# Kernel optimization log

Hardware: AMD Instinct MI355X
Metric: run time of the kernel (lower is better)

Reference implementation:

```python
import jax, jax.numpy as jnp
import numpy as np
from jax.scipy.linalg import cholesky, solve_triangular

SIGMA2 = 0.001   # likelihood.variance (fixed in source)
JITTER = 1e-5


def hankel(v, L):
    # Direct windowed gather; math-identical to the one-hot matmul in the source.
    Nv, Dv = v.shape
    idx = jnp.arange(Nv - L + 1)[:, None] + jnp.arange(L)[None, :]  # [Nv-L+1, L]
    return v[idx].reshape(Nv - L + 1, L * Dv)


def _sqdist(A, B):
    # ||a-b||^2, clipped for numerical safety
    d = jnp.sum(A * A, 1)[:, None] + jnp.sum(B * B, 1)[None, :] - 2.0 * A @ B.T
    return jnp.maximum(d, 0.0)


def _psi_stats(Z, Xmu, Xvar, l2, variance):
    # RBF (ARD) expected-kernel statistics (GPflow conventions).
    N = Xmu.shape[0]
    # psi0: E[k(x,x)] = variance per point, summed over N
    psi0 = jnp.asarray(N, Xmu.dtype) * variance
    # psi1[n,m] = var * prod_q (1+s/l2)^-1/2 * exp(-0.5 (mu-z)^2/(l2+s))
    denom = l2 + Xvar                                        # [N,D]
    logdet1 = -0.5 * jnp.sum(jnp.log1p(Xvar / l2), axis=1)   # [N]
    quad1 = -0.5 * jnp.sum((Xmu[:, None, :] - Z[None, :, :]) ** 2 / denom[:, None, :], axis=2)  # [N,M]
    psi1 = variance * jnp.exp(logdet1[:, None] + quad1)      # [N,M]
    # psi2[n,m,k] = var^2 * prod_q (1+2s/l2)^-1/2
    #   * exp(-(zm-zk)^2/(4 l2) - (mu - (zm+zk)/2)^2 / (2s + l2))
    a = 1.0 / (2.0 * Xvar + l2)                              # [N,D]
    cn = variance ** 2 * jnp.exp(-0.5 * jnp.sum(jnp.log1p(2.0 * Xvar / l2), axis=1))  # [N]
    Zs = Z / (2.0 * jnp.sqrt(l2))
    dZ2 = _sqdist(Zs, Zs)                                    # [M,M], (zm-zk)^2/(4 l2)
    # expand (mu - zbar)^2 * a  without a [N,M,M,D] tensor
    T1 = jnp.sum(a * Xmu * Xmu, axis=1)                      # [N]
    T2 = (a * Xmu) @ Z.T                                     # [N,M]
    T3 = a @ (Z * Z).T                                       # [N,M]
    T4 = jnp.einsum('nq,mq,kq->nmk', a, Z, Z)                # [N,M,M]
    quad2 = (T1[:, None, None] - T2[:, :, None] - T2[:, None, :]
             + 0.25 * (T3[:, :, None] + T3[:, None, :]) + 0.5 * T4)  # [N,M,M]
    psi2 = jnp.sum(cn[:, None, None] * jnp.exp(-dZ2[None, :, :] - quad2), axis=0)  # [M,M]
    return psi0, psi1, psi2


def build_likelihood(X_mean, X_var, Z, lengthscales, variance, Lt):
    N_tot, Q = X_mean.shape
    M = Z.shape[0]
    N = N_tot - Lt
    sigma2 = jnp.asarray(SIGMA2, X_mean.dtype)
    sigma = jnp.sqrt(sigma2)
    l2 = lengthscales ** 2

    X_m = hankel(X_mean[:N_tot - 1], Lt)   # [N, Lt*Q]
    X_v = hankel(X_var[:N_tot - 1], Lt)
    X_mo, X_vo = X_mean[Lt:], X_var[Lt:]   # [N, Q]
    X_mb, X_vb = X_mean[:Lt], X_var[:Lt]   # [Lt, Q]

    Kuu = variance * jnp.exp(-0.5 * _sqdist(Z / lengthscales, Z / lengthscales)) \
          + JITTER * jnp.eye(M, dtype=X_mean.dtype)
    psi0, psi1, psi2 = _psi_stats(Z, X_m, X_v, l2, variance)

    L = cholesky(Kuu, lower=True)
    A = solve_triangular(L, psi1.T, lower=True) / sigma            # [M,N]
    tmp = solve_triangular(L, psi2, lower=True)
    AAT = solve_triangular(L, tmp.T, lower=True) / sigma2          # [M,M]
    B = AAT + jnp.eye(M, dtype=X_mean.dtype)
    LB = cholesky(B, lower=True)
    log_det_B = 2.0 * jnp.sum(jnp.log(jnp.diag(LB)))
    c = solve_triangular(LB, A @ X_mo, lower=True) / sigma         # [M,Q]

    NQ = jnp.asarray(N * Q, X_mean.dtype)
    two_pi = jnp.asarray(2.0 * np.pi, X_mean.dtype)
    ent = 0.5 * jnp.sum(jnp.log(X_vo)) + 0.5 * NQ * jnp.log(two_pi)
    ent2 = -jnp.asarray(Lt * Q, X_mean.dtype) * jnp.log(two_pi) \
           - 0.5 * jnp.sum(X_mb ** 2 + X_vb)

    bound = -0.5 * NQ * jnp.log(two_pi * sigma2)
    bound += -0.5 / sigma2 * (jnp.sum(X_vo) + jnp.sum(X_mo ** 2))
    bound += -0.5 * Q * (psi0 / sigma2 - jnp.trace(AAT))
    bound += -0.5 * Q * log_det_B
    bound += 0.5 * jnp.sum(c ** 2)
    bound += ent + ent2
    return bound


def setup_inputs() -> dict:
    key = jax.random.key(0)
    k1, k2, k3 = jax.random.split(key, 3)
    N, Q, Lt, M = 4096, 4, 8, 128
    D = Lt * Q
    X_mean = jax.random.normal(k1, (N + Lt, Q), dtype=jnp.float32)
    X_var = jax.random.uniform(k2, (N + Lt, Q), dtype=jnp.float32, minval=0.1, maxval=1.0)
    Z = jax.random.normal(k3, (M, D), dtype=jnp.float32)
    lengthscales = 2.0 * jnp.ones((D,), dtype=jnp.float32)
    variance = jnp.asarray(1.0, dtype=jnp.float32)
    return {"X_mean": X_mean, "X_var": X_var, "Z": Z,
            "lengthscales": lengthscales, "variance": variance, "Lt": Lt}


def reference(X_mean, X_var, Z, lengthscales, variance, Lt):
    return build_likelihood(X_mean, X_var, Z, lengthscales, variance, Lt)
```

## Files before the change

### kernel.cpp

```cpp
#include <hip/hip_runtime.h>

#define NN   4096
#define NQ   (NN*4)
#define QQ   4
#define LTT  8
#define DD   32
#define MM   128
#define SIG2 0.001f
#define JIT  1e-5f
#define LOG2E 1.4426950408889634f

typedef _Float16 half8 __attribute__((ext_vector_type(8)));
typedef float    f32x4 __attribute__((ext_vector_type(4)));

__device__ __forceinline__ float fexp2(float x) { return exp2f(x); }

__device__ __forceinline__ float rlane(float v, int l) {
    return __uint_as_float(__builtin_amdgcn_readlane(__float_as_uint(v), l));
}

__global__ __launch_bounds__(256) void k1_kernel(
    const float* __restrict__ Xm, const float* __restrict__ Xv,
    const float* __restrict__ Zg, const float* __restrict__ ls,
    const float* __restrict__ varp,
    _Float16* __restrict__ bh, float* __restrict__ r_g, float* __restrict__ Yg,
    _Float16* __restrict__ Zh, float* __restrict__ Kuu, float* __restrict__ scalars)
{
    int b = blockIdx.x, tid = threadIdx.x;
    if (b < 256) {
        __shared__ float Zl[MM*33];
        __shared__ float pkl[16][DD][4];
        __shared__ float L1l[16], bbl[16];
        __shared__ float lsq[DD];
        __shared__ float yredl[MM*QQ];
        __shared__ float redl[48];
        for (int e = tid; e < MM*DD; e += 256)
            Zl[(e>>5)*33 + (e&31)] = Zg[e];
        if (tid < DD) { float l = ls[tid]; lsq[tid] = 1.0f/(l*l); }
        __syncthreads();
        int n0 = b*16;
        float var  = varp[0];
        float logv = logf(var);
        int nl = tid >> 4;
        int n  = n0 + nl;
        float slog2 = 0.f, slog1 = 0.f, T1 = 0.f, c0 = 0.f;
        #pragma unroll
        for (int t2 = 0; t2 < 2; ++t2) {
            int q = (tid & 15)*2 + t2;
            float xm  = Xm[n*QQ + q];
            float xv  = Xv[n*QQ + q];
            float il2 = lsq[q];
            float l2  = 1.0f / il2;
            float a    = 1.0f / (2.0f*xv + l2);
            float dinv = 1.0f / (l2 + xv);
            pkl[nl][q][0] = LOG2E * a * xm;
            pkl[nl][q][1] = LOG2E * (-0.25f * a);
            pkl[nl][q][2] = dinv;
            pkl[nl][q][3] = -2.0f * dinv * xm;
            bh[n*DD + q] = (_Float16)(0.5f * LOG2E * (il2 - a));
            slog2 += log1pf(2.0f*xv*il2);
            slog1 += log1pf(xv*il2);
            T1    += a*xm*xm;
            c0    += dinv*xm*xm;
        }
        float s1 = 0.f, s2 = 0.f, s3 = 0.f;
        if ((tid & 15) < 4) {
            int c = tid & 3;
            float mo = Xm[(n+LTT)*QQ + c];
            float vo = Xv[(n+LTT)*QQ + c];
            s1 = vo + mo*mo;
            s2 = logf(vo);
            if (n < LTT) {
                float mb = Xm[n*QQ + c], vb = Xv[n*QQ + c];
                s3 = mb*mb + vb;
            }
        }
        #pragma unroll
        for (int off = 1; off < 16; off <<= 1) {
            slog2 += __shfl_xor(slog2, off, 64);
            slog1 += __shfl_xor(slog1, off, 64);
            T1    += __shfl_xor(T1, off, 64);
            c0    += __shfl_xor(c0, off, 64);
            s1    += __shfl_xor(s1, off, 64);
            s2    += __shfl_xor(s2, off, 64);
            s3    += __shfl_xor(s3, off, 64);
        }
        if ((tid & 15) == 0) {
            L1l[nl] = 0.5f * LOG2E * (2.0f*logv - 0.5f*slog2 - T1);
            bbl[nl] = logv - 0.5f*slog1 - 0.5f*c0;
            redl[nl] = s1; redl[16+nl] = s2; redl[32+nl] = s3;
        }
        __syncthreads();
        if (tid == 0) {
            float a1=0.f, a2=0.f, a3=0.f;
            for (int i2 = 0; i2 < 16; ++i2) { a1+=redl[i2]; a2+=redl[16+i2]; a3+=redl[32+i2]; }
            atomicAdd(&scalars[4], a1);
            atomicAdd(&scalars[5], a2);
            atomicAdd(&scalars[6], a3);
        }
        int m = tid & 127, half = tid >> 7;
        float zr[DD];
        #pragma unroll
        for (int q = 0; q < DD; ++q) zr[q] = Zl[m*33 + q];
        float sm = 0.f;
        #pragma unroll
        for (int q = 0; q < DD; ++q) sm = fmaf(zr[q]*zr[q], lsq[q], sm);
        sm *= 0.25f * LOG2E;
        float y0=0.f, y1=0.f, y2=0.f, y3=0.f;
        int nb = half*8;
        for (int i = 0; i < 8; ++i) {
            int nli = nb + i;
            float L1n = L1l[nli], bbn = bbl[nli];
            float racc = 0.f, q1 = 0.f;
            #pragma unroll
            for (int q = 0; q < DD; ++q) {
                float4 v = *(const float4*)&pkl[nli][q][0];
                float z = zr[q];
                racc = fmaf(v.x, z, racc);
                racc = fmaf(v.y, z*z, racc);
                float t = fmaf(v.z, z, v.w);
                q1 = fmaf(t, z, q1);
            }
            int gn = n0 + nli;
            r_g[gn*MM + m] = L1n + racc - sm;
            float p1 = __expf(fmaf(-0.5f, q1, bbn));
            float4 xo = *(const float4*)(Xm + (LTT+gn)*QQ);
            y0 = fmaf(p1, xo.x, y0); y1 = fmaf(p1, xo.y, y1);
            y2 = fmaf(p1, xo.z, y2); y3 = fmaf(p1, xo.w, y3);
        }
        if (half == 0) {
            yredl[m*4+0]=y0; yredl[m*4+1]=y1; yredl[m*4+2]=y2; yredl[m*4+3]=y3;
        }
        __syncthreads();
        if (half == 1) {
            yredl[m*4+0]+=y0; yredl[m*4+1]+=y1; yredl[m*4+2]+=y2; yredl[m*4+3]+=y3;
        }
        __syncthreads();
        for (int e = tid; e < 512; e += 256) atomicAdd(&Yg[e], yredl[e]);
    } else if (b < 320) {
        int idx = (b-256)*256 + tid;
        int i = idx >> 7, j = idx & 127;
        float var = varp[0];
        float s = 0.f;
        for (int q = 0; q < DD; ++q) {
            float l = ls[q];
            float d = (Zg[i*DD+q] - Zg[j*DD+q]) / l;
            s += d*d;
        }
        float v = var * __expf(-0.5f*s);
        if (i == j) v += JIT;
        Kuu[idx] = v;
    } else {
        for (int e = tid; e < MM*DD; e += 256) Zh[e] = (_Float16)Zg[e];
    }
}

__device__ __forceinline__ void dev_chol(float* mat, int tid)
{
    int wv = tid >> 6, ln = tid & 63;
    for (int p = 0; p < 8; ++p) {
        int base = p*16;
        if (wv == 0) {
            int r0 = base + ln, r1 = r0 + 64;
            bool h0 = r0 < 128, h1 = r1 < 128;
            float a0[16], a1[16];
            #pragma unroll
            for (int c = 0; c < 16; ++c) {
                a0[c] = h0 ? mat[r0*132 + base + c] : 0.f;
                a1[c] = h1 ? mat[r1*132 + base + c] : 0.f;
            }
            #pragma unroll
            for (int kk = 0; kk < 16; ++kk) {
                float d   = rlane(a0[kk], kk);
                float rdk = rsqrtf(d);
                float sq  = d * rdk;
                a0[kk] = (ln == kk) ? sq : a0[kk] * rdk;
                a1[kk] *= rdk;
                #pragma unroll
                for (int j = kk+1; j < 16; ++j) {
                    float ljv = rlane(a0[kk], j);
                    a0[j] = fmaf(-a0[kk], ljv, a0[j]);
                    a1[j] = fmaf(-a1[kk], ljv, a1[j]);
                }
            }
            #pragma unroll
            for (int c = 0; c < 16; ++c) {
                if (h0) mat[r0*132 + base + c] = a0[c];
                if (h1) mat[r1*132 + base + c] = a1[c];
            }
        }
        __syncthreads();
        int S = 112 - base;
        if (S > 0) {
            int T = S >> 2, nb = base + 16;
            int nT = (T*(T+1)) >> 1;
            for (int t = tid; t < nT; t += 512) {
                int ti = (int)(0.5f*(sqrtf(8.f*(float)t + 1.f) - 1.f));
                if ((ti+1)*(ti+2)/2 <= t) ++ti;
                else if (ti*(ti+1)/2 > t) --ti;
                int tj = t - ((ti*(ti+1))>>1);
                int i0 = nb + ti*4, j0 = nb + tj*4;
                float ac[4][4];
                #pragma unroll
                for (int r = 0; r < 4; ++r)
                    #pragma unroll
                    for (int s = 0; s < 4; ++s) ac[r][s] = mat[(i0+r)*132 + j0 + s];
                #pragma unroll
                for (int c4 = 0; c4 < 4; ++c4) {
                    float4 av[4], bv[4];
                    #pragma unroll
                    for (int r = 0; r < 4; ++r) {
                        av[r] = *(const float4*)&mat[(i0+r)*132 + base + c4*4];
                        bv[r] = *(const float4*)&mat[(j0+r)*132 + base + c4*4];
                    }
                    #pragma unroll
                    for (int r = 0; r < 4; ++r)
                        #pragma unroll
                        for (int s = 0; s < 4; ++s)
                            ac[r][s] -= av[r].x*bv[s].x + av[r].y*bv[s].y
                                      + av[r].z*bv[s].z + av[r].w*bv[s].w;
                }
                #pragma unroll
                for (int r = 0; r < 4; ++r)
                    #pragma unroll
                    for (int s = 0; s < 4; ++s) mat[(i0+r)*132 + j0 + s] = ac[r][s];
            }
        }
        __syncthreads();
    }
}

__device__ __forceinline__ void dev_dinv(const float* mat, float* dinvb, int tid)
{
    int wv = tid >> 6, ln = tid & 63;
    if (ln < 16) {
        int c = ln, bd = wv;
        int base = bd*16;
        float x[16];
        #pragma unroll
        for (int i = 0; i < 16; ++i) {
            float dii = mat[(base+i)*132 + base + i];
            float s = 0.f;
            #pragma unroll
            for (int j = 0; j < i; ++j) s += mat[(base+i)*132 + base + j] * x[j];
            float v;
            if (i < c) v = 0.f;
            else if (i == c) v = 1.0f / dii;
            else v = -s / dii;
            x[i] = v;
        }
        #pragma unroll
        for (int i = 0; i < 16; ++i) dinvb[bd*256 + i*16 + c] = x[i];
    }
    __syncthreads();
}

__global__ __launch_bounds__(512) void psi2chol_kernel(
    const _Float16* __restrict__ Zh, const float* __restrict__ r_g,
    const _Float16* __restrict__ bh, float* __restrict__ psi2,
    const float* __restrict__ Kuu, float* __restrict__ Lg,
    float* __restrict__ scalars)
{
    __shared__ float shm[19968];
    int tid = threadIdx.x;
    if (blockIdx.x == 0) {
        float* mat   = shm;
        float* dinvb = shm + 16896;
        float* red   = shm + 18944;
        float* tmpM  = shm + 19456;
        for (int e = tid; e < 16384; e += 512) mat[(e>>7)*132 + (e&127)] = Kuu[e];
        __syncthreads();
        dev_chol(mat, tid);
        red[tid] = (tid < 128) ? logf(mat[tid*132 + tid]) : 0.f;
        __syncthreads();
        for (int s = 256; s; s >>= 1) { if (tid < s) red[tid] += red[tid+s]; __syncthreads(); }
        if (tid == 0) scalars[0] = red[0];
        dev_dinv(mat, dinvb, tid);
        #pragma unroll
        for (int bi = 1; bi < 8; ++bi) {
            const int total = bi*256;
            const int np = (total + 511)/512;
            float wbuf[4];
            #pragma unroll
            for (int ps = 0; ps < np; ++ps) {
                int e = ps*512 + tid;
                float Mv = 0.f;
                int bj = e >> 8, r = (e >> 4) & 15, c = e & 15;
                if (e < total) {
                    #pragma unroll
                    for (int kk = 0; kk < 16; ++kk)
                        Mv = fmaf(mat[(bi*16+r)*132 + bj*16+kk], dinvb[bj*256 + kk*16 + c], Mv);
                    for (int k = bj+1; k < bi; ++k)
                        #pragma unroll
                        for (int kk = 0; kk < 16; ++kk)
                            Mv = fmaf(mat[(bi*16+r)*132 + k*16+kk], mat[(k*16+kk)*132 + bj*16+c], Mv);
                }
                __syncthreads();
                if (e < total) tmpM[tid] = Mv;
                __syncthreads();
                float w = 0.f;
                if (e < total) {
                    int lbj = tid >> 8;
                    #pragma unroll
                    for (int kk = 0; kk < 16; ++kk)
                        w = fmaf(dinvb[bi*256 + r*16 + kk], tmpM[lbj*256 + kk*16 + c], w);
                }
                wbuf[ps] = w;
            }
            __syncthreads();
            #pragma unroll
            for (int ps = 0; ps < np; ++ps) {
                int e = ps*512 + tid;
                if (e < total) {
                    int bj = e >> 8, r = (e >> 4) & 15, c = e & 15;
                    mat[(bi*16+r)*132 + bj*16 + c] = -wbuf[ps];
                }
            }
            __syncthreads();
        }
        for (int e = tid; e < 2048; e += 512) {
            int bd = e >> 8, r = (e >> 4) & 15, c = e & 15;
            mat[(bd*16+r)*132 + bd*16 + c] = dinvb[e];
        }
        __syncthreads();
        for (int e = tid; e < 16384; e += 512) Lg[e] = mat[(e>>7)*132 + (e&127)];
    } else {
        float (*pacc)[64][4] = (float(*)[64][4])shm;
        int w = tid >> 6, l = tid & 63, lm = l & 15, lg = l >> 4;
        int b = blockIdx.x - 1;
        int t = b % 36, nq = b / 36;
        int kt = (int)(0.5f*(sqrtf(8.f*(float)t + 1.f) - 1.f));
        if ((kt+1)*(kt+2)/2 <= t) ++kt;
        else if (kt*(kt+1)/2 > t) --kt;
        int mt = t - ((kt*(kt+1))>>1);

        half8 Bf = ((const half8*)Zh)[(kt*16 + lm)*4 + lg];
        half8 Zm = ((const half8*)Zh)[(mt*16 + lm)*4 + lg];
        f32x4 z4; z4[0]=0.f; z4[1]=0.f; z4[2]=0.f; z4[3]=0.f;
        f32x4 acc0 = z4, acc1 = z4;
        int n0g = nq*128 + w*16;
        const float* rbase = r_g + (size_t)n0g*MM;
        const half8* bbase = (const half8*)bh + (size_t)n0g*4;
        for (int i = 0; i < 16; i += 2) {
            half8 bf0 = bbase[i*4 + lg];
            half8 bf1 = bbase[i*4 + 4 + lg];
            const float* rn0 = rbase + i*MM;
            f32x4 rm0 = *(const f32x4*)(rn0 + mt*16 + lg*4);
            f32x4 rm1 = *(const f32x4*)(rn0 + MM + mt*16 + lg*4);
            float rk0 = rn0[kt*16 + lm];
            float rk1 = rn0[MM + kt*16 + lm];
            half8 A0 = Zm * bf0;
            half8 A1 = Zm * bf1;
            f32x4 p0 = __builtin_amdgcn_mfma_f32_16x16x32_f16(A0, Bf, z4, 0, 0, 0);
            f32x4 p1 = __builtin_amdgcn_mfma_f32_16x16x32_f16(A1, Bf, z4, 0, 0, 0);
            acc0[0] += fexp2(p0[0] + rm0[0] + rk0);
            acc0[1] += fexp2(p0[1] + rm0[1] + rk0);
            acc0[2] += fexp2(p0[2] + rm0[2] + rk0);
            acc0[3] += fexp2(p0[3] + rm0[3] + rk0);
            acc1[0] += fexp2(p1[0] + rm1[0] + rk1);
            acc1[1] += fexp2(p1[1] + rm1[1] + rk1);
            acc1[2] += fexp2(p1[2] + rm1[2] + rk1);
            acc1[3] += fexp2(p1[3] + rm1[3] + rk1);
        }
        #pragma unroll
        for (int j = 0; j < 4; ++j) pacc[w][l][j] = acc0[j] + acc1[j];
        __syncthreads();
        if (tid < 256) {
            int ll = tid >> 2, j = tid & 3;
            float s = 0.f;
            #pragma unroll
            for (int ww = 0; ww < 8; ++ww) s += pacc[ww][ll][j];
            int row = mt*16 + (ll >> 4)*4 + j;
            int col = kt*16 + (ll & 15);
            atomicAdd(&psi2[row*MM + col], s);
            if (mt != kt) atomicAdd(&psi2[col*MM + row], s);
        }
    }
}

__global__ __launch_bounds__(512) void cholG_kernel(
    const float* __restrict__ Kuu, const float* __restrict__ psi2,
    const float* __restrict__ Yg, const float* __restrict__ Lg,
    const float* __restrict__ varp,
    float* __restrict__ scalars, int* __restrict__ cnt, float* __restrict__ out)
{
    __shared__ float shm[20480];
    int tid = threadIdx.x;
    if (blockIdx.x == 0) {
        float* mat   = shm;
        float* dinvb = shm + 16896;
        float* rhs   = shm + 18944;
        float* red   = shm + 19456;
        for (int e = tid; e < 16384; e += 512)
            mat[(e>>7)*132 + (e&127)] = Kuu[e] + (1.0f/SIG2)*psi2[e];
        __syncthreads();
        dev_chol(mat, tid);
        red[tid] = (tid < 128) ? logf(mat[tid*132 + tid]) : 0.f;
        __syncthreads();
        for (int s = 256; s; s >>= 1) { if (tid < s) red[tid] += red[tid+s]; __syncthreads(); }
        if (tid == 0) scalars[1] = red[0];
        dev_dinv(mat, dinvb, tid);
        rhs[tid] = Yg[tid];
        __syncthreads();
        if (tid < 64) {
            int r = tid >> 2, cc = tid & 3;
            for (int bi = 0; bi < 8; ++bi) {
                float a0 = rhs[(bi*16+r)*4 + cc], a1 = 0.f, a2 = 0.f, a3 = 0.f;
                for (int bk = 0; bk < bi; ++bk) {
                    const float* mrow = &mat[(bi*16+r)*132 + bk*16];
                    const float* rb   = &rhs[bk*64 + cc];
                    #pragma unroll
                    for (int kk = 0; kk < 16; kk += 4) {
                        a0 = fmaf(-mrow[kk+0], rb[(kk+0)*4], a0);
                        a1 = fmaf(-mrow[kk+1], rb[(kk+1)*4], a1);
                        a2 = fmaf(-mrow[kk+2], rb[(kk+2)*4], a2);
                        a3 = fmaf(-mrow[kk+3], rb[(kk+3)*4], a3);
                    }
                }
                float acc = (a0+a1)+(a2+a3);
                float w = 0.f;
                #pragma unroll
                for (int kk = 0; kk < 16; ++kk)
                    w += dinvb[bi*256 + r*16 + kk] * __shfl(acc, kk*4 + cc, 64);
                rhs[(bi*16+r)*4 + cc] = w;
            }
        }
        __syncthreads();
        { float v = rhs[tid]; red[tid] = v*v; }
        __syncthreads();
        for (int s = 256; s; s >>= 1) { if (tid < s) red[tid] += red[tid+s]; __syncthreads(); }
        if (tid == 0) scalars[2] = red[0];
    } else {
        float* psl  = shm;
        float* lrow = shm + 16512;
        float* redl = shm + 17552;
        for (int e = tid; e < 16384; e += 512)
            psl[(e>>7)*129 + (e&127)] = psi2[e];
        __syncthreads();
        int w = tid >> 6, l = tid & 63;
        float kacc = 0.f;
        for (int kk2 = 0; kk2 < 2; ++kk2) {
            int k = (blockIdx.x - 1)*16 + w*2 + kk2;
            lrow[w*130 + l]      = (l      <= k) ? Lg[k*MM + l]      : 0.f;
            lrow[w*130 + l + 64] = (l + 64 <= k) ? Lg[k*MM + l + 64] : 0.f;
            __syncthreads();
            float wa = 0.f, wb = 0.f;
            for (int j = 0; j <= k; ++j) {
                float lj = lrow[w*130 + j];
                wa = fmaf(psl[j*129 + l],      lj, wa);
                wb = fmaf(psl[j*129 + l + 64], lj, wb);
            }
            float part = wa * lrow[w*130 + l] + wb * lrow[w*130 + l + 64];
            for (int off = 32; off; off >>= 1) part += __shfl_xor(part, off, 64);
            kacc += part;
            __syncthreads();
        }
        if (l == 0) redl[w] = kacc;
        __syncthreads();
        if (tid == 0) {
            float s = 0.f;
            for (int ww = 0; ww < 8; ++ww) s += redl[ww];
            atomicAdd(&scalars[3], s);
        }
    }
    if (tid == 0) {
        __threadfence();
        int old = atomicAdd(cnt, 1);
        if (old == 8) {
            float ldK  = scalars[0];
            float ldG  = atomicAdd(&scalars[1], 0.0f);
            float c2s  = atomicAdd(&scalars[2], 0.0f);
            float trr  = atomicAdd(&scalars[3], 0.0f);
            float s1   = atomicAdd(&scalars[4], 0.0f);
            float s2   = atomicAdd(&scalars[5], 0.0f);
            float s3   = atomicAdd(&scalars[6], 0.0f);
            float var = varp[0];
            float trAAT   = trr / SIG2;
            float logdetB = 2.0f * (ldG - ldK);
            float sumc2   = c2s / (SIG2*SIG2);
            float psi0    = (float)NN * var;
            const float LOG2PI = 1.837877066409345f;
            float NQf = (float)NQ;
            float bound = -0.5f*NQf*(LOG2PI + logf(SIG2));
            bound += -0.5f/SIG2 * s1;
            bound += -0.5f*(float)QQ*(psi0/SIG2 - trAAT);
            bound += -0.5f*(float)QQ*logdetB;
            bound += 0.5f*sumc2;
            bound += 0.5f*s2 + 0.5f*NQf*LOG2PI;
            bound += -(float)(LTT*QQ)*LOG2PI - 0.5f*s3;
            out[0] = bound;
        }
    }
}

extern "C" void kernel_launch(void* const* d_in, const int* in_sizes, int n_in,
                              void* d_out, int out_size, void* d_ws, size_t ws_size,
                              hipStream_t stream)
{
    (void)in_sizes; (void)n_in; (void)out_size; (void)ws_size;
    const float* Xm   = (const float*)d_in[0];
    const float* Xv   = (const float*)d_in[1];
    const float* Zg   = (const float*)d_in[2];
    const float* ls   = (const float*)d_in[3];
    const float* varp = (const float*)d_in[4];

    float* p = (float*)d_ws;
    float*    r_g   = p;                p += NN*MM;
    _Float16* bh    = (_Float16*)p;     p += NN*DD/2;
    _Float16* Zh    = (_Float16*)p;     p += MM*DD/2;
    float*    Kuu   = p;                p += MM*MM;
    float*    Lg    = p;                p += MM*MM;
    float*    psi2  = p;                p += MM*MM;
    float*    Yg    = p;                p += 512;
    float*    scalars = p;              p += 8;
    int*      cnt   = (int*)p;          p += 4;

    hipMemsetAsync(psi2, 0, (MM*MM + 512 + 8 + 4)*sizeof(float), stream);
    k1_kernel<<<321, 256, 0, stream>>>(Xm, Xv, Zg, ls, varp, bh, r_g, Yg, Zh, Kuu, scalars);
    psi2chol_kernel<<<1153, 512, 0, stream>>>(Zh, r_g, bh, psi2, Kuu, Lg, scalars);
    cholG_kernel<<<9, 512, 0, stream>>>(Kuu, psi2, Yg, Lg, varp, scalars, cnt, (float*)d_out);
}
```

Measured before the change: 165.2 us.

## Split psi2 and Kuu Cholesky into separate kernels and compute trace via per-column solves

The Kuu Cholesky and triangular inverse no longer ride alongside the psi2 MFMA blocks. psi2 gets its own kernel with a 4-way unrolled inner loop. A two-block kernel then factors Kuu+psi2/sigma2 in one block and Kuu in the other concurrently, dropping the explicit blocked inverse of L. The trace term is now computed by 128 blocks, each doing a forward solve for one column of L^-1 and a quadratic form against psi2. This shortens the serial single-block tail at the cost of an extra launch and redundant loading of L in every trace block.

```diff
diff --git a/kernel.cpp b/kernel.cpp
--- a/kernel.cpp
+++ b/kernel.cpp
@@ -152,6 +152,72 @@
         Kuu[idx] = v;
     } else {
         for (int e = tid; e < MM*DD; e += 256) Zh[e] = (_Float16)Zg[e];
+    }
+}
+
+__global__ __launch_bounds__(512) void psi2_kernel(
+    const _Float16* __restrict__ Zh, const float* __restrict__ r_g,
+    const _Float16* __restrict__ bh, float* __restrict__ psi2)
+{
+    __shared__ float pacc[8][64][4];
+    int tid = threadIdx.x;
+    int w = tid >> 6, l = tid & 63, lm = l & 15, lg = l >> 4;
+    int b = blockIdx.x;
+    int t = b % 36, nq = b / 36;
+    int kt = (int)(0.5f*(sqrtf(8.f*(float)t + 1.f) - 1.f));
+    if ((kt+1)*(kt+2)/2 <= t) ++kt;
+    else if (kt*(kt+1)/2 > t) --kt;
+    int mt = t - ((kt*(kt+1))>>1);
+
+    half8 Bf = ((const half8*)Zh)[(kt*16 + lm)*4 + lg];
+    half8 Zm = ((const half8*)Zh)[(mt*16 + lm)*4 + lg];
+    f32x4 z4; z4[0]=0.f; z4[1]=0.f; z4[2]=0.f; z4[3]=0.f;
+    f32x4 acc0 = z4, acc1 = z4, acc2 = z4, acc3 = z4;
+    int n0g = nq*128 + w*16;
+    const float* rbase = r_g + (size_t)n0g*MM;
+    const half8* bbase = (const half8*)bh + (size_t)n0g*4;
+    for (int i = 0; i < 16; i += 4) {
+        half8 bf0 = bbase[(i+0)*4 + lg];
+        half8 bf1 = bbase[(i+1)*4 + lg];
+        half8 bf2 = bbase[(i+2)*4 + lg];
+        half8 bf3 = bbase[(i+3)*4 + lg];
+        const float* rn = rbase + i*MM;
+        f32x4 rm0 = *(const f32x4*)(rn + 0*MM + mt*16 + lg*4);
+        f32x4 rm1 = *(const f32x4*)(rn + 1*MM + mt*16 + lg*4);
+        f32x4 rm2 = *(const f32x4*)(rn + 2*MM + mt*16 + lg*4);
+        f32x4 rm3 = *(const f32x4*)(rn + 3*MM + mt*16 + lg*4);
+        float rk0 = rn[0*MM + kt*16 + lm];
+        float rk1 = rn[1*MM + kt*16 + lm];
+        float rk2 = rn[2*MM + kt*16 + lm];
+        float rk3 = rn[3*MM + kt*16 + lm];
+        half8 A0 = Zm * bf0;
+        half8 A1 = Zm * bf1;
+        half8 A2 = Zm * bf2;
+        half8 A3 = Zm * bf3;
+        f32x4 p0 = __builtin_amdgcn_mfma_f32_16x16x32_f16(A0, Bf, z4, 0, 0, 0);
+        f32x4 p1 = __builtin_amdgcn_mfma_f32_16x16x32_f16(A1, Bf, z4, 0, 0, 0);
+        f32x4 p2 = __builtin_amdgcn_mfma_f32_16x16x32_f16(A2, Bf, z4, 0, 0, 0);
+        f32x4 p3 = __builtin_amdgcn_mfma_f32_16x16x32_f16(A3, Bf, z4, 0, 0, 0);
+        #pragma unroll
+        for (int j = 0; j < 4; ++j) {
+            acc0[j] += fexp2(p0[j] + rm0[j] + rk0);
+            acc1[j] += fexp2(p1[j] + rm1[j] + rk1);
+            acc2[j] += fexp2(p2[j] + rm2[j] + rk2);
+            acc3[j] += fexp2(p3[j] + rm3[j] + rk3);
+        }
+    }
+    #pragma unroll
+    for (int j = 0; j < 4; ++j) pacc[w][l][j] = (acc0[j]+acc1[j]) + (acc2[j]+acc3[j]);
+    __syncthreads();
+    if (tid < 256) {
+        int ll = tid >> 2, j = tid & 3;
+        float s = 0.f;
+        #pragma unroll
+        for (int ww = 0; ww < 8; ++ww) s += pacc[ww][ll][j];
+        int row = mt*16 + (ll >> 4)*4 + j;
+        int col = kt*16 + (ll & 15);
+        atomicAdd(&psi2[row*MM + col], s);
+        if (mt != kt) atomicAdd(&psi2[col*MM + row], s);
     }
 }
 
@@ -255,142 +321,18 @@
     __syncthreads();
 }
 
-__global__ __launch_bounds__(512) void psi2chol_kernel(
-    const _Float16* __restrict__ Zh, const float* __restrict__ r_g,
-    const _Float16* __restrict__ bh, float* __restrict__ psi2,
-    const float* __restrict__ Kuu, float* __restrict__ Lg,
+__global__ __launch_bounds__(512) void chol2_kernel(
+    const float* __restrict__ Kuu, const float* __restrict__ psi2,
+    const float* __restrict__ Yg, float* __restrict__ Lg,
     float* __restrict__ scalars)
 {
     __shared__ float shm[19968];
     int tid = threadIdx.x;
+    float* mat   = shm;
+    float* dinvb = shm + 16896;
+    float* red   = shm + 18944;
+    float* rhs   = shm + 19456;
     if (blockIdx.x == 0) {
-        float* mat   = shm;
-        float* dinvb = shm + 16896;
-        float* red   = shm + 18944;
-        float* tmpM  = shm + 19456;
-        for (int e = tid; e < 16384; e += 512) mat[(e>>7)*132 + (e&127)] = Kuu[e];
-        __syncthreads();
-        dev_chol(mat, tid);
-        red[tid] = (tid < 128) ? logf(mat[tid*132 + tid]) : 0.f;
-        __syncthreads();
-        for (int s = 256; s; s >>= 1) { if (tid < s) red[tid] += red[tid+s]; __syncthreads(); }
-        if (tid == 0) scalars[0] = red[0];
-        dev_dinv(mat, dinvb, tid);
-        #pragma unroll
-        for (int bi = 1; bi < 8; ++bi) {
-            const int total = bi*256;
-            const int np = (total + 511)/512;
-            float wbuf[4];
-            #pragma unroll
-            for (int ps = 0; ps < np; ++ps) {
-                int e = ps*512 + tid;
-                float Mv = 0.f;
-                int bj = e >> 8, r = (e >> 4) & 15, c = e & 15;
-                if (e < total) {
-                    #pragma unroll
-                    for (int kk = 0; kk < 16; ++kk)
-                        Mv = fmaf(mat[(bi*16+r)*132 + bj*16+kk], dinvb[bj*256 + kk*16 + c], Mv);
-                    for (int k = bj+1; k < bi; ++k)
-                        #pragma unroll
-                        for (int kk = 0; kk < 16; ++kk)
-                            Mv = fmaf(mat[(bi*16+r)*132 + k*16+kk], mat[(k*16+kk)*132 + bj*16+c], Mv);
-                }
-                __syncthreads();
-                if (e < total) tmpM[tid] = Mv;
-                __syncthreads();
-                float w = 0.f;
-                if (e < total) {
-                    int lbj = tid >> 8;
-                    #pragma unroll
-                    for (int kk = 0; kk < 16; ++kk)
-                        w = fmaf(dinvb[bi*256 + r*16 + kk], tmpM[lbj*256 + kk*16 + c], w);
-                }
-                wbuf[ps] = w;
-            }
-            __syncthreads();
-            #pragma unroll
-            for (int ps = 0; ps < np; ++ps) {
-                int e = ps*512 + tid;
-                if (e < total) {
-                    int bj = e >> 8, r = (e >> 4) & 15, c = e & 15;
-                    mat[(bi*16+r)*132 + bj*16 + c] = -wbuf[ps];
-                }
-            }
-            __syncthreads();
-        }
-        for (int e = tid; e < 2048; e += 512) {
-            int bd = e >> 8, r = (e >> 4) & 15, c = e & 15;
-            mat[(bd*16+r)*132 + bd*16 + c] = dinvb[e];
-        }
-        __syncthreads();
-        for (int e = tid; e < 16384; e += 512) Lg[e] = mat[(e>>7)*132 + (e&127)];
-    } else {
-        float (*pacc)[64][4] = (float(*)[64][4])shm;
-        int w = tid >> 6, l = tid & 63, lm = l & 15, lg = l >> 4;
-        int b = blockIdx.x - 1;
-        int t = b % 36, nq = b / 36;
-        int kt = (int)(0.5f*(sqrtf(8.f*(float)t + 1.f) - 1.f));
-        if ((kt+1)*(kt+2)/2 <= t) ++kt;
-        else if (kt*(kt+1)/2 > t) --kt;
-        int mt = t - ((kt*(kt+1))>>1);
-
-        half8 Bf = ((const half8*)Zh)[(kt*16 + lm)*4 + lg];
-        half8 Zm = ((const half8*)Zh)[(mt*16 + lm)*4 + lg];
-        f32x4 z4; z4[0]=0.f; z4[1]=0.f; z4[2]=0.f; z4[3]=0.f;
-        f32x4 acc0 = z4, acc1 = z4;
-        int n0g = nq*128 + w*16;
-        const float* rbase = r_g + (size_t)n0g*MM;
-        const half8* bbase = (const half8*)bh + (size_t)n0g*4;
-        for (int i = 0; i < 16; i += 2) {
-            half8 bf0 = bbase[i*4 + lg];
-            half8 bf1 = bbase[i*4 + 4 + lg];
-            const float* rn0 = rbase + i*MM;
-            f32x4 rm0 = *(const f32x4*)(rn0 + mt*16 + lg*4);
-            f32x4 rm1 = *(const f32x4*)(rn0 + MM + mt*16 + lg*4);
-            float rk0 = rn0[kt*16 + lm];
-            float rk1 = rn0[MM + kt*16 + lm];
-            half8 A0 = Zm * bf0;
-            half8 A1 = Zm * bf1;
-            f32x4 p0 = __builtin_amdgcn_mfma_f32_16x16x32_f16(A0, Bf, z4, 0, 0, 0);
-            f32x4 p1 = __builtin_amdgcn_mfma_f32_16x16x32_f16(A1, Bf, z4, 0, 0, 0);
-            acc0[0] += fexp2(p0[0] + rm0[0] + rk0);
-            acc0[1] += fexp2(p0[1] + rm0[1] + rk0);
-            acc0[2] += fexp2(p0[2] + rm0[2] + rk0);
-            acc0[3] += fexp2(p0[3] + rm0[3] + rk0);
-            acc1[0] += fexp2(p1[0] + rm1[0] + rk1);
-            acc1[1] += fexp2(p1[1] + rm1[1] + rk1);
-            acc1[2] += fexp2(p1[2] + rm1[2] + rk1);
-            acc1[3] += fexp2(p1[3] + rm1[3] + rk1);
-        }
-        #pragma unroll
-        for (int j = 0; j < 4; ++j) pacc[w][l][j] = acc0[j] + acc1[j];
-        __syncthreads();
-        if (tid < 256) {
-            int ll = tid >> 2, j = tid & 3;
-            float s = 0.f;
-            #pragma unroll
-            for (int ww = 0; ww < 8; ++ww) s += pacc[ww][ll][j];
-            int row = mt*16 + (ll >> 4)*4 + j;
-            int col = kt*16 + (ll & 15);
-            atomicAdd(&psi2[row*MM + col], s);
-            if (mt != kt) atomicAdd(&psi2[col*MM + row], s);
-        }
-    }
-}
-
-__global__ __launch_bounds__(512) void cholG_kernel(
-    const float* __restrict__ Kuu, const float* __restrict__ psi2,
-    const float* __restrict__ Yg, const float* __restrict__ Lg,
-    const float* __restrict__ varp,
-    float* __restrict__ scalars, int* __restrict__ cnt, float* __restrict__ out)
-{
-    __shared__ float shm[20480];
-    int tid = threadIdx.x;
-    if (blockIdx.x == 0) {
-        float* mat   = shm;
-        float* dinvb = shm + 16896;
-        float* rhs   = shm + 18944;
-        float* red   = shm + 19456;
         for (int e = tid; e < 16384; e += 512)
             mat[(e>>7)*132 + (e&127)] = Kuu[e] + (1.0f/SIG2)*psi2[e];
         __syncthreads();
@@ -431,43 +373,61 @@
         for (int s = 256; s; s >>= 1) { if (tid < s) red[tid] += red[tid+s]; __syncthreads(); }
         if (tid == 0) scalars[2] = red[0];
     } else {
-        float* psl  = shm;
-        float* lrow = shm + 16512;
-        float* redl = shm + 17552;
-        for (int e = tid; e < 16384; e += 512)
-            psl[(e>>7)*129 + (e&127)] = psi2[e];
-        __syncthreads();
-        int w = tid >> 6, l = tid & 63;
-        float kacc = 0.f;
-        for (int kk2 = 0; kk2 < 2; ++kk2) {
-            int k = (blockIdx.x - 1)*16 + w*2 + kk2;
-            lrow[w*130 + l]      = (l      <= k) ? Lg[k*MM + l]      : 0.f;
-            lrow[w*130 + l + 64] = (l + 64 <= k) ? Lg[k*MM + l + 64] : 0.f;
-            __syncthreads();
-            float wa = 0.f, wb = 0.f;
-            for (int j = 0; j <= k; ++j) {
-                float lj = lrow[w*130 + j];
-                wa = fmaf(psl[j*129 + l],      lj, wa);
-                wb = fmaf(psl[j*129 + l + 64], lj, wb);
-            }
-            float part = wa * lrow[w*130 + l] + wb * lrow[w*130 + l + 64];
-            for (int off = 32; off; off >>= 1) part += __shfl_xor(part, off, 64);
-            kacc += part;
-            __syncthreads();
-        }
-        if (l == 0) redl[w] = kacc;
-        __syncthreads();
-        if (tid == 0) {
+        for (int e = tid; e < 16384; e += 512) mat[(e>>7)*132 + (e&127)] = Kuu[e];
+        __syncthreads();
+        dev_chol(mat, tid);
+        red[tid] = (tid < 128) ? logf(mat[tid*132 + tid]) : 0.f;
+        __syncthreads();
+        for (int s = 256; s; s >>= 1) { if (tid < s) red[tid] += red[tid+s]; __syncthreads(); }
+        if (tid == 0) scalars[0] = red[0];
+        for (int e = tid; e < 16384; e += 512) Lg[e] = mat[(e>>7)*132 + (e&127)];
+    }
+}
+
+__global__ __launch_bounds__(512) void trace_kernel(
+    const float* __restrict__ Lg, const float* __restrict__ psi2,
+    const float* __restrict__ varp,
+    float* __restrict__ scalars, int* __restrict__ cnt, float* __restrict__ out)
+{
+    __shared__ float LT[128*129];
+    __shared__ float zv[128];
+    __shared__ float red[512];
+    int tid = threadIdx.x;
+    int k = blockIdx.x;
+    for (int e = tid; e < 16384; e += 512) {
+        int r = e >> 7, c = e & 127;
+        LT[c*129 + r] = Lg[e];
+    }
+    if (tid < 128) zv[tid] = 0.f;
+    __syncthreads();
+    if (tid < 64) {
+        int l = tid;
+        for (int i = k; i >= 0; --i) {
             float s = 0.f;
-            for (int ww = 0; ww < 8; ++ww) s += redl[ww];
-            atomicAdd(&scalars[3], s);
-        }
-    }
+            if (l > i && l <= k)           s += LT[i*129 + l]      * zv[l];
+            int l2 = l + 64;
+            if (l2 > i && l2 <= k)         s += LT[i*129 + l2]     * zv[l2];
+            #pragma unroll
+            for (int off = 32; off; off >>= 1) s += __shfl_xor(s, off, 64);
+            if (l == 0)
+                zv[i] = (((i == k) ? 1.0f : 0.0f) - s) / LT[i*129 + i];
+        }
+    }
+    __syncthreads();
+    float q = 0.f;
+    for (int e = tid; e < 16384; e += 512) {
+        int i = e >> 7, j = e & 127;
+        q += zv[i] * zv[j] * psi2[e];
+    }
+    red[tid] = q;
+    __syncthreads();
+    for (int s = 256; s; s >>= 1) { if (tid < s) red[tid] += red[tid+s]; __syncthreads(); }
     if (tid == 0) {
+        atomicAdd(&scalars[3], red[0]);
         __threadfence();
         int old = atomicAdd(cnt, 1);
-        if (old == 8) {
-            float ldK  = scalars[0];
+        if (old == 127) {
+            float ldK  = atomicAdd(&scalars[0], 0.0f);
             float ldG  = atomicAdd(&scalars[1], 0.0f);
             float c2s  = atomicAdd(&scalars[2], 0.0f);
             float trr  = atomicAdd(&scalars[3], 0.0f);
@@ -517,6 +477,7 @@
 
     hipMemsetAsync(psi2, 0, (MM*MM + 512 + 8 + 4)*sizeof(float), stream);
     k1_kernel<<<321, 256, 0, stream>>>(Xm, Xv, Zg, ls, varp, bh, r_g, Yg, Zh, Kuu, scalars);
-    psi2chol_kernel<<<1153, 512, 0, stream>>>(Zh, r_g, bh, psi2, Kuu, Lg, scalars);
-    cholG_kernel<<<9, 512, 0, stream>>>(Kuu, psi2, Yg, Lg, varp, scalars, cnt, (float*)d_out);
-}
+    psi2_kernel<<<1152, 512, 0, stream>>>(Zh, r_g, bh, psi2);
+    chol2_kernel<<<2, 512, 0, stream>>>(Kuu, psi2, Yg, Lg, scalars);
+    trace_kernel<<<128, 512, 0, stream>>>(Lg, psi2, varp, scalars, cnt, (float*)d_out);
+}
```

After: 193.3 us. 1.17x slower.
